# Performance work log

Measured on AMD Instinct MI355X. Metric: run time of the kernel, lower is better.

Reference implementation:

```python
import jax, jax.numpy as jnp
import numpy as np

D_MODEL = 1024
D_STATE = 16
D_CONV = 4
EXPAND = 2
D_INNER = EXPAND * D_MODEL
DT_RANK = (D_MODEL + 15) // 16  # ceil(d_model/16) = 64
BATCH = 2
SEQLEN = 1024


def _causal_conv_silu(x, w, b):
    # x: (B, d_inner, L); w: (d_inner, 1, k) depthwise; causal left padding k-1
    k = w.shape[-1]
    y = jax.lax.conv_general_dilated(
        x, w, window_strides=(1,), padding=[(k - 1, 0)],
        dimension_numbers=("NCH", "OIH", "NCH"), feature_group_count=x.shape[1])
    return jax.nn.silu(y + b[None, :, None])


def _ssm_scan(dA, dBx):
    # h_t = dA_t * h_{t-1} + dBx_t, parallel associative scan over L (axis=2)
    def op(e1, e2):
        a1, b1 = e1
        a2, b2 = e2
        return (a1 * a2, a2 * b1 + b2)
    return jax.lax.associative_scan(op, (dA, dBx), axis=2)[1]


def _mamba_dir(xz, conv_w, conv_b, xproj_w, dtproj_w, dt_bias, A_log, Dp):
    d_inner = xz.shape[1] // 2
    x, z = xz[:, :d_inner], xz[:, d_inner:]
    u = _causal_conv_silu(x, conv_w, conv_b)                  # (B, d, L)
    x_dbl = jnp.einsum('bdl,kd->bkl', u, xproj_w)             # (B, dt_rank+2n, L)
    n = A_log.shape[1]
    r = dtproj_w.shape[1]
    delta = jnp.einsum('dr,brl->bdl', dtproj_w, x_dbl[:, :r])
    Bm = x_dbl[:, r:r + n]                                    # (B, n, L)
    Cm = x_dbl[:, r + n:]                                     # (B, n, L)
    delta = jax.nn.softplus(delta + dt_bias[None, :, None])
    A = -jnp.exp(A_log)                                       # (d, n)
    dA = jnp.exp(jnp.einsum('bdl,dn->bdln', delta, A))
    dBx = jnp.einsum('bdl,bnl,bdl->bdln', delta, Bm, u)
    h = _ssm_scan(dA, dBx)                                    # (B, d, L, n)
    y = jnp.einsum('bdln,bnl->bdl', h, Cm)
    y = y + Dp[None, :, None] * u
    return y * jax.nn.silu(z)


def setup_inputs() -> dict:
    key = jax.random.key(0)
    ks = jax.random.split(key, 16)
    s_in = 1.0 / np.sqrt(D_MODEL)
    s_x = 1.0 / np.sqrt(D_INNER)
    dt_std = DT_RANK ** -0.5

    def dt_bias_init(k):
        dt = jnp.exp(jax.random.uniform(k, (D_INNER,)) * (np.log(0.1) - np.log(0.001)) + np.log(0.001))
        dt = jnp.clip(dt, 1e-4, None)
        return dt + jnp.log(-jnp.expm1(-dt))  # inverse softplus

    A_log = jnp.log(jnp.tile(jnp.arange(1, D_STATE + 1, dtype=jnp.float32)[None, :], (D_INNER, 1)))
    inp = {
        'hidden_states': jax.random.normal(ks[0], (BATCH, SEQLEN, D_MODEL), jnp.float32),
        'in_proj_w': jax.random.normal(ks[1], (2 * D_INNER, D_MODEL), jnp.float32) * s_in,
        'conv_w': jax.random.normal(ks[2], (D_INNER, 1, D_CONV), jnp.float32) * 0.3,
        'conv_bias': jnp.zeros((D_INNER,), jnp.float32),
        'x_proj_w': jax.random.normal(ks[3], (DT_RANK + 2 * D_STATE, D_INNER), jnp.float32) * s_x,
        'dt_proj_w': jax.random.uniform(ks[4], (D_INNER, DT_RANK), jnp.float32, -dt_std, dt_std),
        'dt_proj_bias': dt_bias_init(ks[5]),
        'A_log': A_log,
        'D_skip': jnp.ones((D_INNER,), jnp.float32),
        'convb_w': jax.random.normal(ks[6], (D_INNER, 1, D_CONV), jnp.float32) * 0.3,
        'convb_bias': jnp.zeros((D_INNER,), jnp.float32),
        'x_proj_b_w': jax.random.normal(ks[7], (DT_RANK + 2 * D_STATE, D_INNER), jnp.float32) * s_x,
        'dt_proj_b_w': jax.random.uniform(ks[8], (D_INNER, DT_RANK), jnp.float32, -dt_std, dt_std),
        'dt_proj_b_bias': dt_bias_init(ks[9]),
        'A_b_log': A_log,
        'D_b_skip': jnp.ones((D_INNER,), jnp.float32),
        'out_proj_w': jax.random.normal(ks[10], (D_MODEL, D_INNER), jnp.float32) * s_x,
    }
    return inp


def reference(hidden_states, in_proj_w, conv_w, conv_bias, x_proj_w, dt_proj_w,
              dt_proj_bias, A_log, D_skip, convb_w, convb_bias, x_proj_b_w,
              dt_proj_b_w, dt_proj_b_bias, A_b_log, D_b_skip, out_proj_w):
    # in_proj (no bias): (B, 2*d_inner, L)
    xz = jnp.einsum('ed,bld->bel', in_proj_w, hidden_states)
    out_f = _mamba_dir(xz, conv_w, conv_bias, x_proj_w, dt_proj_w, dt_proj_bias, A_log, D_skip)
    out_b = _mamba_dir(xz[:, :, ::-1], convb_w, convb_bias, x_proj_b_w, dt_proj_b_w,
                       dt_proj_b_bias, A_b_log, D_b_skip)[:, :, ::-1]
    # if_divide_out=False: just sum then out_proj (no bias)
    return jnp.einsum('bdl,od->blo', out_f + out_b, out_proj_w)
```

## Files before the change

### kernel.cpp

```cpp
#include <hip/hip_runtime.h>
#include <math.h>


typedef _Float16 f16x8 __attribute__((ext_vector_type(8)));
typedef _Float16 f16x4 __attribute__((ext_vector_type(4)));
typedef float    f32x4 __attribute__((ext_vector_type(4)));

#define SCH 16
#define SCL 64

__device__ __forceinline__ void gload_lds16(const void* g, void* l) {
    __builtin_amdgcn_global_load_lds(
        (const __attribute__((address_space(1))) void*)g,
        (__attribute__((address_space(3))) void*)l, 16, 0, 0);
}

__device__ __forceinline__ float softplus_f(float x) {
    float e = __builtin_amdgcn_exp2f(-fabsf(x) * 1.44269504f);
    return fmaxf(x, 0.f) + __builtin_amdgcn_logf(1.f + e) * 0.69314718f;
}

template<int CTRL>
__device__ __forceinline__ float dpp_add(float x) {
    int s = __builtin_amdgcn_update_dpp(0, __builtin_bit_cast(int, x),
                                        CTRL, 0xF, 0xF, true);
    return x + __builtin_bit_cast(float, s);
}

template<int WMW, int WNW, int FM, int FN>
__global__ __launch_bounds__(256)
void gemm_nt_f16(const _Float16* __restrict__ A, const _Float16* __restrict__ B,
                 float* __restrict__ C, int K, int ldc, long sA, long sC)
{
    constexpr int BM = WMW * FM * 16, BN = WNW * FN * 16;
    constexpr int ACH = BM / 8, NCH = (BM + BN) / 8;
    __shared__ __align__(16) _Float16 lds[(BM + BN) * 64];
    A += (long)blockIdx.z * sA;
    C += (long)blockIdx.z * sC;
    const int m0 = blockIdx.y * BM, n0 = blockIdx.x * BN;
    const int t = threadIdx.x, wid = t >> 6, lane = t & 63;
    const int wm = wid / WNW, wn = wid % WNW;
    const int srow = lane >> 3;
    const int skk  = ((lane & 7) ^ srow) * 8;

    f32x4 acc[FM][FN];
#pragma unroll
    for (int i = 0; i < FM; ++i)
#pragma unroll
        for (int j = 0; j < FN; ++j) acc[i][j] = (f32x4){0.f, 0.f, 0.f, 0.f};

    for (int k0 = 0; k0 < K; k0 += 64) {
#pragma unroll
        for (int c = wid; c < NCH; c += 4) {
            const _Float16* gp = (c < ACH)
                ? A + (long)(m0 + c * 8 + srow) * K + k0 + skk
                : B + (long)(n0 + (c - ACH) * 8 + srow) * K + k0 + skk;
            gload_lds16(gp, lds + c * 512);
        }
        __syncthreads();
#pragma unroll
        for (int kw = 0; kw < 2; ++kw) {
            f16x8 af[FM], bf[FN];
#pragma unroll
            for (int i = 0; i < FM; ++i) {
                int r = wm * FM * 16 + i * 16 + (lane & 15);
                af[i] = *(const f16x8*)(lds + r * 64 +
                        (((kw * 4 + (lane >> 4)) ^ (r & 7)) * 8));
            }
#pragma unroll
            for (int j = 0; j < FN; ++j) {
                int r = wn * FN * 16 + j * 16 + (lane & 15);
                bf[j] = *(const f16x8*)(lds + BM * 64 + r * 64 +
                        (((kw * 4 + (lane >> 4)) ^ (r & 7)) * 8));
            }
#pragma unroll
            for (int i = 0; i < FM; ++i)
#pragma unroll
                for (int j = 0; j < FN; ++j)
                    acc[i][j] = __builtin_amdgcn_mfma_f32_16x16x32_f16(
                        af[i], bf[j], acc[i][j], 0, 0, 0);
        }
        __syncthreads();
    }
#pragma unroll
    for (int i = 0; i < FM; ++i)
#pragma unroll
        for (int j = 0; j < FN; ++j) {
            int n = n0 + wn * FN * 16 + j * 16 + (lane & 15);
            int m = m0 + wm * FM * 16 + i * 16 + (lane >> 4) * 4;
            *(f32x4*)&C[(long)n * ldc + m] = acc[i][j];
        }
}

#define XP_SK 8
__global__ __launch_bounds__(256)
void xproj_f16_kernel(const float* __restrict__ u, const _Float16* __restrict__ xw16,
                      float* __restrict__ pb)
{
    __shared__ __align__(16) _Float16 Asw[128 * 64];
    __shared__ __align__(16) _Float16 Bsw[96 * 64];
    const int t = threadIdx.x, wid = t >> 6, lane = t & 63;
    const int wm = wid >> 1, wn = wid & 1;
    const int m0 = blockIdx.x * 128;
    const int sk = blockIdx.y, dirb = blockIdx.z;
    const float* ub = u + (long)dirb * 2048 * 1024;
    const _Float16* Bw = xw16 + (long)(dirb >> 1) * 96 * 2048;
    const int srow = lane >> 3;
    const int skk  = ((lane & 7) ^ srow) * 8;
    const int lloc = (t & 31) * 4;
    const int kslt = t >> 5;

    f32x4 acc[4][3];
#pragma unroll
    for (int i = 0; i < 4; ++i)
#pragma unroll
        for (int j = 0; j < 3; ++j) acc[i][j] = (f32x4){0.f, 0.f, 0.f, 0.f};

    for (int ks = 0; ks < 2048 / XP_SK; ks += 64) {
        const int k0 = sk * (2048 / XP_SK) + ks;
#pragma unroll
        for (int c = wid; c < 12; c += 4)
            gload_lds16(Bw + (long)(c * 8 + srow) * 2048 + k0 + skk, Bsw + c * 512);
        float av[8][4];
#pragma unroll
        for (int kk = 0; kk < 8; ++kk) {
            f32x4 v = *(const f32x4*)&ub[(long)(k0 + kslt * 8 + kk) * 1024 + m0 + lloc];
            av[kk][0] = v.x; av[kk][1] = v.y; av[kk][2] = v.z; av[kk][3] = v.w;
        }
#pragma unroll
        for (int q = 0; q < 4; ++q) {
            int l = lloc + q;
            f16x8 h = {(_Float16)av[0][q], (_Float16)av[1][q], (_Float16)av[2][q],
                       (_Float16)av[3][q], (_Float16)av[4][q], (_Float16)av[5][q],
                       (_Float16)av[6][q], (_Float16)av[7][q]};
            *(f16x8*)(Asw + l * 64 + ((kslt ^ (l & 7)) * 8)) = h;
        }
        __syncthreads();
#pragma unroll
        for (int kw = 0; kw < 2; ++kw) {
            f16x8 af[4], bf[3];
#pragma unroll
            for (int i = 0; i < 4; ++i) {
                int r = wm * 64 + i * 16 + (lane & 15);
                af[i] = *(const f16x8*)(Asw + r * 64 +
                        (((kw * 4 + (lane >> 4)) ^ (r & 7)) * 8));
            }
#pragma unroll
            for (int j = 0; j < 3; ++j) {
                int r = wn * 48 + j * 16 + (lane & 15);
                bf[j] = *(const f16x8*)(Bsw + r * 64 +
                        (((kw * 4 + (lane >> 4)) ^ (r & 7)) * 8));
            }
#pragma unroll
            for (int i = 0; i < 4; ++i)
#pragma unroll
                for (int j = 0; j < 3; ++j)
                    acc[i][j] = __builtin_amdgcn_mfma_f32_16x16x32_f16(
                        af[i], bf[j], acc[i][j], 0, 0, 0);
        }
        __syncthreads();
    }
    float* Cp = pb + ((long)sk * 4 + dirb) * 96 * 1024;
#pragma unroll
    for (int i = 0; i < 4; ++i)
#pragma unroll
        for (int j = 0; j < 3; ++j) {
            int n = wn * 48 + j * 16 + (lane & 15);
            int m = m0 + wm * 64 + i * 16 + (lane >> 4) * 4;
            *(f32x4*)&Cp[(long)n * 1024 + m] = acc[i][j];
        }
}

__global__ __launch_bounds__(256)
void xreduce_kernel(const float* __restrict__ pb, float* __restrict__ xdbl)
{
    int f = (blockIdx.x * 256 + threadIdx.x) * 4;
    f32x4 s = (f32x4){0.f, 0.f, 0.f, 0.f};
#pragma unroll
    for (int sk = 0; sk < XP_SK; ++sk)
        s += *(const f32x4*)(pb + (long)sk * 393216 + f);
    *(f32x4*)(xdbl + f) = s;
}

__global__ __launch_bounds__(256)
void dtproj_f16_kernel(const float* __restrict__ xdbl, const _Float16* __restrict__ dw16,
                       const float* __restrict__ bcat, float* __restrict__ delta)
{
    __shared__ __align__(16) _Float16 Asw[128 * 64];
    __shared__ __align__(16) _Float16 Bsw[128 * 64];
    const int t = threadIdx.x, wid = t >> 6, lane = t & 63;
    const int wm = wid >> 1, wn = wid & 1;
    const int n0 = blockIdx.x * 128, m0 = blockIdx.y * 128;
    const int dirb = blockIdx.z, dir = dirb >> 1;
    const float* Xb = xdbl + (long)dirb * 96 * 1024;
    const _Float16* Bw = dw16 + (long)dir * 2048 * 64;
    const int srow = lane >> 3, skk = ((lane & 7) ^ srow) * 8;
    const int lloc = (t & 31) * 4, kslt = t >> 5;

#pragma unroll
    for (int c = wid; c < 16; c += 4)
        gload_lds16(Bw + (long)(n0 + c * 8 + srow) * 64 + skk, Bsw + c * 512);
    float av[8][4];
#pragma unroll
    for (int kk = 0; kk < 8; ++kk) {
        f32x4 v = *(const f32x4*)&Xb[(long)(kslt * 8 + kk) * 1024 + m0 + lloc];
        av[kk][0] = v.x; av[kk][1] = v.y; av[kk][2] = v.z; av[kk][3] = v.w;
    }
#pragma unroll
    for (int q = 0; q < 4; ++q) {
        int l = lloc + q;
        f16x8 h = {(_Float16)av[0][q], (_Float16)av[1][q], (_Float16)av[2][q],
                   (_Float16)av[3][q], (_Float16)av[4][q], (_Float16)av[5][q],
                   (_Float16)av[6][q], (_Float16)av[7][q]};
        *(f16x8*)(Asw + l * 64 + ((kslt ^ (l & 7)) * 8)) = h;
    }
    __syncthreads();

    f32x4 acc[4][4];
#pragma unroll
    for (int i = 0; i < 4; ++i)
#pragma unroll
        for (int j = 0; j < 4; ++j) acc[i][j] = (f32x4){0.f, 0.f, 0.f, 0.f};
#pragma unroll
    for (int kw = 0; kw < 2; ++kw) {
        f16x8 af[4], bf[4];
#pragma unroll
        for (int i = 0; i < 4; ++i) {
            int r = wm * 64 + i * 16 + (lane & 15);
            af[i] = *(const f16x8*)(Asw + r * 64 +
                    (((kw * 4 + (lane >> 4)) ^ (r & 7)) * 8));
        }
#pragma unroll
        for (int j = 0; j < 4; ++j) {
            int r = wn * 64 + j * 16 + (lane & 15);
            bf[j] = *(const f16x8*)(Bsw + r * 64 +
                    (((kw * 4 + (lane >> 4)) ^ (r & 7)) * 8));
        }
#pragma unroll
        for (int i = 0; i < 4; ++i)
#pragma unroll
            for (int j = 0; j < 4; ++j)
                acc[i][j] = __builtin_amdgcn_mfma_f32_16x16x32_f16(
                    af[i], bf[j], acc[i][j], 0, 0, 0);
    }
    float* Dp = delta + (long)dirb * 2048 * 1024;
#pragma unroll
    for (int j = 0; j < 4; ++j) {
        int dd = n0 + wn * 64 + j * 16 + (lane & 15);
        float bm = bcat[dir * 2048 + dd];
#pragma unroll
        for (int i = 0; i < 4; ++i) {
            int m = m0 + wm * 64 + i * 16 + (lane >> 4) * 4;
            f32x4 v = acc[i][j];
            f32x4 o = {softplus_f(v.x + bm), softplus_f(v.y + bm),
                       softplus_f(v.z + bm), softplus_f(v.w + bm)};
            *(f32x4*)&Dp[(long)dd * 1024 + m] = o;
        }
    }
}

__global__ __launch_bounds__(256)
void cvt_f16_kernel(const float* __restrict__ in, _Float16* __restrict__ out, int n)
{
    int i = (blockIdx.x * 256 + threadIdx.x) * 4;
    if (i + 3 < n) {
        float4 v = *(const float4*)(in + i);
        f16x4 h = {(_Float16)v.x, (_Float16)v.y, (_Float16)v.z, (_Float16)v.w};
        *(f16x4*)(out + i) = h;
    }
}

__global__ __launch_bounds__(256)
void concat_weights(const float* __restrict__ xwf, const float* __restrict__ xwb,
                    const float* __restrict__ dwf, const float* __restrict__ dwb,
                    const float* __restrict__ bf,  const float* __restrict__ bb,
                    _Float16* __restrict__ xw16, _Float16* __restrict__ dw16,
                    float* __restrict__ bcat)
{
    int i = blockIdx.x * 256 + threadIdx.x;
    if (i < 196608) { xw16[i] = (_Float16)xwf[i]; xw16[196608 + i] = (_Float16)xwb[i]; }
    if (i < 131072) { dw16[i] = (_Float16)dwf[i]; dw16[131072 + i] = (_Float16)dwb[i]; }
    if (i < 2048)   { bcat[i]  = bf[i];  bcat[2048 + i] = bb[i]; }
}

__global__ __launch_bounds__(256)
void conv_silu_kernel(const float* __restrict__ xz,
                      const float* __restrict__ wf, const float* __restrict__ bf,
                      const float* __restrict__ wb, const float* __restrict__ bbk,
                      float* __restrict__ u)
{
    long idx = (long)blockIdx.x * 256 + threadIdx.x;
    int l = (int)(idx & 1023);
    long r = idx >> 10;
    int d = (int)(r & 2047);
    int b = (int)((r >> 11) & 1);
    int dir = (int)(r >> 12);
    const float* x = xz + ((long)b * 4096 + d) * 1024;
    const float* w = dir ? wb : wf;
    float s = dir ? bbk[d] : bf[d];
    if (dir == 0) {
#pragma unroll
        for (int j = 0; j < 4; ++j) {
            int p = l - 3 + j;
            if (p >= 0) s = fmaf(w[d * 4 + j], x[p], s);
        }
    } else {
#pragma unroll
        for (int j = 0; j < 4; ++j) {
            int src = l - 3 + j;
            if (src >= 0) s = fmaf(w[d * 4 + j], x[1023 - src], s);
        }
    }
    u[idx] = s / (1.f + __builtin_amdgcn_exp2f(-s * 1.44269504f));
}

__global__ __launch_bounds__(256)
void scan_p1_kernel(const float* __restrict__ u, const float* __restrict__ delta,
                    const float* __restrict__ xdbl,
                    const float* __restrict__ Alf, const float* __restrict__ Alb,
                    float* __restrict__ hend, float* __restrict__ aprod)
{
    __shared__ float sD[64][66], sU[64][66], sB[64][20];
    const int t = threadIdx.x, wid = t >> 6, lane = t & 63;
    const int nl = lane & 3;
    const int dloc = wid * 16 + (lane >> 2);
    const int dblk = blockIdx.x, chunk = blockIdx.y, dirb = blockIdx.z;
    const int d = dblk * 64 + dloc, dir = dirb >> 1;
    const int T0 = chunk * SCL;
    f32x4 Av = *(const f32x4*)((dir ? Alb : Alf) + d * 16 + nl * 4);
    float An2[4] = {-expf(Av.x) * 1.44269504f, -expf(Av.y) * 1.44269504f,
                    -expf(Av.z) * 1.44269504f, -expf(Av.w) * 1.44269504f};
    const float* dp = delta + ((long)dirb * 2048 + dblk * 64) * 1024;
    const float* up = u     + ((long)dirb * 2048 + dblk * 64) * 1024;
    const float* Bp = xdbl  + ((long)dirb * 96 + 64) * 1024;

#pragma unroll
    for (int rep = 0; rep < 4; ++rep) {
        int ii = rep * 256 + t;
        int dd = ii >> 4, q = ii & 15;
        *(f32x4*)&sD[dd][q * 4] = *(const f32x4*)&dp[(long)dd * 1024 + T0 + q * 4];
        *(f32x4*)&sU[dd][q * 4] = *(const f32x4*)&up[(long)dd * 1024 + T0 + q * 4];
    }
#pragma unroll
    for (int rep = 0; rep < 4; ++rep) {
        int ii = rep * 256 + t;
        int n = ii >> 6, tt = ii & 63;
        sB[tt][n] = Bp[(long)n * 1024 + T0 + tt];
    }
    __syncthreads();

    float h[4] = {0.f, 0.f, 0.f, 0.f};
    float S = 0.f;
#pragma unroll 4
    for (int g = 0; g < 16; ++g) {
        f32x4 dlv = *(const f32x4*)&sD[dloc][g * 4];
        f32x4 uuv = *(const f32x4*)&sU[dloc][g * 4];
        float dls[4] = {dlv.x, dlv.y, dlv.z, dlv.w};
        float uus[4] = {uuv.x, uuv.y, uuv.z, uuv.w};
#pragma unroll
        for (int r4 = 0; r4 < 4; ++r4) {
            f32x4 Bv = *(const f32x4*)&sB[g * 4 + r4][nl * 4];
            float Bs[4] = {Bv.x, Bv.y, Bv.z, Bv.w};
            float dl = dls[r4], t1 = dl * uus[r4];
            S += dl;
#pragma unroll
            for (int r = 0; r < 4; ++r)
                h[r] = fmaf(__builtin_amdgcn_exp2f(dl * An2[r]), h[r], t1 * Bs[r]);
        }
    }
    long cb = (((long)dirb * SCH + chunk) * 2048 + d) * 16 + nl * 4;
    *(f32x4*)&hend[cb]  = (f32x4){h[0], h[1], h[2], h[3]};
    *(f32x4*)&aprod[cb] = (f32x4){__builtin_amdgcn_exp2f(S * An2[0]),
                                  __builtin_amdgcn_exp2f(S * An2[1]),
                                  __builtin_amdgcn_exp2f(S * An2[2]),
                                  __builtin_amdgcn_exp2f(S * An2[3])};
}

__global__ __launch_bounds__(256)
void scan_carry_kernel(const float* __restrict__ hend, const float* __restrict__ aprod,
                       float* __restrict__ hinit)
{
    int f = blockIdx.x * 256 + threadIdx.x;
    int dn = f & 32767;
    int dirb = f >> 15;
    long base = (long)dirb * SCH * 32768 + dn;
    float hcur = 0.f;
#pragma unroll
    for (int c = 0; c < SCH; ++c) {
        hinit[base + (long)c * 32768] = hcur;
        hcur = hend[base + (long)c * 32768]
             + aprod[base + (long)c * 32768] * hcur;
    }
}

__global__ __launch_bounds__(256)
void scan_p3_kernel(const float* __restrict__ u, const float* __restrict__ delta,
                    const float* __restrict__ xdbl,
                    const float* __restrict__ Alf, const float* __restrict__ Alb,
                    const float* __restrict__ Df, const float* __restrict__ Db,
                    const float* __restrict__ hinit, float* __restrict__ y)
{
    __shared__ float sD[64][66], sU[64][66], sB[64][20], sC[64][20];
    const int t = threadIdx.x, wid = t >> 6, lane = t & 63;
    const int nl = lane & 3;
    const int dloc = wid * 16 + (lane >> 2);
    const int dblk = blockIdx.x, chunk = blockIdx.y, dirb = blockIdx.z;
    const int d = dblk * 64 + dloc, dir = dirb >> 1;
    const int T0 = chunk * SCL;
    f32x4 Av = *(const f32x4*)((dir ? Alb : Alf) + d * 16 + nl * 4);
    float An2[4] = {-expf(Av.x) * 1.44269504f, -expf(Av.y) * 1.44269504f,
                    -expf(Av.z) * 1.44269504f, -expf(Av.w) * 1.44269504f};
    const float Dd = (dir ? Db : Df)[d];
    const float* dp = delta + ((long)dirb * 2048 + dblk * 64) * 1024;
    const float* up = u     + ((long)dirb * 2048 + dblk * 64) * 1024;
    const float* Bp = xdbl  + ((long)dirb * 96 + 64) * 1024;
    const float* Cp = xdbl  + ((long)dirb * 96 + 80) * 1024;
    float* yrow = y + ((long)dirb * 2048 + d) * 1024;

#pragma unroll
    for (int rep = 0; rep < 4; ++rep) {
        int ii = rep * 256 + t;
        int dd = ii >> 4, q = ii & 15;
        *(f32x4*)&sD[dd][q * 4] = *(const f32x4*)&dp[(long)dd * 1024 + T0 + q * 4];
        *(f32x4*)&sU[dd][q * 4] = *(const f32x4*)&up[(long)dd * 1024 + T0 + q * 4];
    }
#pragma unroll
    for (int rep = 0; rep < 4; ++rep) {
        int ii = rep * 256 + t;
        int n = ii >> 6, tt = ii & 63;
        sB[tt][n] = Bp[(long)n * 1024 + T0 + tt];
        sC[tt][n] = Cp[(long)n * 1024 + T0 + tt];
    }
    long cb = (((long)dirb * SCH + chunk) * 2048 + d) * 16 + nl * 4;
    f32x4 h0v = *(const f32x4*)&hinit[cb];
    float h[4] = {h0v.x, h0v.y, h0v.z, h0v.w};
    const bool m[4] = {nl == 0, nl == 1, nl == 2, nl == 3};
    __syncthreads();

#pragma unroll 4
    for (int g = 0; g < 16; ++g) {
        f32x4 dlv = *(const f32x4*)&sD[dloc][g * 4];
        f32x4 uuv = *(const f32x4*)&sU[dloc][g * 4];
        float dls[4] = {dlv.x, dlv.y, dlv.z, dlv.w};
        float uus[4] = {uuv.x, uuv.y, uuv.z, uuv.w};
        float keep = 0.f;
#pragma unroll
        for (int r4 = 0; r4 < 4; ++r4) {
            f32x4 Bv = *(const f32x4*)&sB[g * 4 + r4][nl * 4];
            f32x4 Cv = *(const f32x4*)&sC[g * 4 + r4][nl * 4];
            float Bs[4] = {Bv.x, Bv.y, Bv.z, Bv.w};
            float Cs[4] = {Cv.x, Cv.y, Cv.z, Cv.w};
            float dl = dls[r4], uu = uus[r4];
            float t1 = dl * uu;
#pragma unroll
            for (int r = 0; r < 4; ++r)
                h[r] = fmaf(__builtin_amdgcn_exp2f(dl * An2[r]), h[r], t1 * Bs[r]);
            float p = h[0] * Cs[0];
            p = fmaf(h[1], Cs[1], p);
            p = fmaf(h[2], Cs[2], p);
            p = fmaf(h[3], Cs[3], p);
            p = dpp_add<0xB1>(p);
            p = dpp_add<0x4E>(p);
            float fy = fmaf(Dd, uu, p);
            keep = m[r4] ? fy : keep;
        }
        yrow[T0 + g * 4 + nl] = keep;
    }
}

__global__ __launch_bounds__(256)
void combine_T_kernel(const float* __restrict__ xz, const float* __restrict__ y,
                      _Float16* __restrict__ GT)
{
    __shared__ float Ls[64][65];
    const int d0 = blockIdx.x * 64, l0 = blockIdx.y * 64, b = blockIdx.z;
    const int t = threadIdx.x;
#pragma unroll
    for (int rep = 0; rep < 4; ++rep) {
        int i = rep * 256 + t;
        int dl = i >> 4;
        int lq = (i & 15) * 4;
        const float* zp  = xz + ((long)b * 4096 + 2048 + d0 + dl) * 1024 + l0 + lq;
        const float* yfp = y  + ((long)(b)     * 2048 + d0 + dl) * 1024 + l0 + lq;
        const float* ybp = y  + ((long)(2 + b) * 2048 + d0 + dl) * 1024 + (1020 - l0 - lq);
        float4 vz = *(const float4*)zp;
        float4 vf = *(const float4*)yfp;
        float4 vb = *(const float4*)ybp;
        float zz[4]  = {vz.x, vz.y, vz.z, vz.w};
        float ff[4]  = {vf.x, vf.y, vf.z, vf.w};
        float bbv[4] = {vb.w, vb.z, vb.y, vb.x};
#pragma unroll
        for (int qq = 0; qq < 4; ++qq) {
            float z = zz[qq];
            float sz = z / (1.f + __builtin_amdgcn_exp2f(-z * 1.44269504f));
            Ls[dl][lq + qq] = sz * (ff[qq] + bbv[qq]);
        }
    }
    __syncthreads();
#pragma unroll
    for (int rep = 0; rep < 4; ++rep) {
        int i = rep * 256 + t;
        int ll = i >> 4;
        int dq = (i & 15) * 4;
        f16x4 h = {(_Float16)Ls[dq][ll], (_Float16)Ls[dq + 1][ll],
                   (_Float16)Ls[dq + 2][ll], (_Float16)Ls[dq + 3][ll]};
        *(f16x4*)(GT + ((long)(b * 1024 + l0 + ll)) * 2048 + d0 + dq) = h;
    }
}

extern "C" void kernel_launch(void* const* d_in, const int* in_sizes, int n_in,
                              void* d_out, int out_size, void* d_ws, size_t ws_size,
                              hipStream_t stream)
{
    const float* hidden   = (const float*)d_in[0];
    const float* inproj_w = (const float*)d_in[1];
    const float* conv_w   = (const float*)d_in[2];
    const float* conv_b   = (const float*)d_in[3];
    const float* xproj_w  = (const float*)d_in[4];
    const float* dtproj_w = (const float*)d_in[5];
    const float* dt_bias  = (const float*)d_in[6];
    const float* A_log    = (const float*)d_in[7];
    const float* D_skip   = (const float*)d_in[8];
    const float* convb_w  = (const float*)d_in[9];
    const float* convb_b  = (const float*)d_in[10];
    const float* xprojb_w = (const float*)d_in[11];
    const float* dtprojb_w= (const float*)d_in[12];
    const float* dtb_bias = (const float*)d_in[13];
    const float* Ab_log   = (const float*)d_in[14];
    const float* Db_skip  = (const float*)d_in[15];
    const float* outproj_w= (const float*)d_in[16];
    float* out = (float*)d_out;

    float* ws    = (float*)d_ws;
    float* xz    = ws;
    float* u     = ws + 8388608;
    float* xdbl  = ws + 16777216;
    float* delta = ws + 17170432;
    float* y     = ws + 25559040;
    _Float16* H16    = (_Float16*)u;
    _Float16* Win16  = (_Float16*)(u + 1048576);
    float*    xpb    = delta;
    _Float16* GT     = (_Float16*)delta;
    _Float16* Wout16 = (_Float16*)y;
    _Float16* dw16   = (_Float16*)y;
    float*    bcat   = y + 131072;
    _Float16* xw16   = (_Float16*)(y + 135168);
    float* hend  = y;
    float* aprod = y + 2097152;
    float* hinit = xz;

    hipLaunchKernelGGL(cvt_f16_kernel, dim3(2048), dim3(256), 0, stream,
        hidden, H16, 2097152);
    hipLaunchKernelGGL(cvt_f16_kernel, dim3(4096), dim3(256), 0, stream,
        inproj_w, Win16, 4194304);

    hipLaunchKernelGGL(concat_weights, dim3(768), dim3(256), 0, stream,
        xproj_w, xprojb_w, dtproj_w, dtprojb_w, dt_bias, dtb_bias,
        xw16, dw16, bcat);

    hipLaunchKernelGGL((gemm_nt_f16<2, 2, 4, 4>),
        dim3(32, 8, 2), dim3(256), 0, stream,
        H16, Win16, xz, 1024, 1024, 1048576L, 4194304L);

    hipLaunchKernelGGL(conv_silu_kernel, dim3(32768), dim3(256), 0, stream,
        xz, conv_w, conv_b, convb_w, convb_b, u);

    hipLaunchKernelGGL(xproj_f16_kernel, dim3(8, XP_SK, 4), dim3(256), 0, stream,
        u, xw16, xpb);
    hipLaunchKernelGGL(xreduce_kernel, dim3(384), dim3(256), 0, stream,
        xpb, xdbl);

    hipLaunchKernelGGL(dtproj_f16_kernel, dim3(16, 8, 4), dim3(256), 0, stream,
        xdbl, dw16, bcat, delta);

    hipLaunchKernelGGL(scan_p1_kernel, dim3(32, SCH, 4), dim3(256), 0, stream,
        u, delta, xdbl, A_log, Ab_log, hend, aprod);
    hipLaunchKernelGGL(scan_carry_kernel, dim3(512), dim3(256), 0, stream,
        hend, aprod, hinit);
    hipLaunchKernelGGL(scan_p3_kernel, dim3(32, SCH, 4), dim3(256), 0, stream,
        u, delta, xdbl, A_log, Ab_log, D_skip, Db_skip, hinit, y);

    hipLaunchKernelGGL(combine_T_kernel, dim3(32, 16, 2), dim3(256), 0, stream,
        xz, y, GT);

    hipLaunchKernelGGL(cvt_f16_kernel, dim3(2048), dim3(256), 0, stream,
        outproj_w, Wout16, 2097152);

    hipLaunchKernelGGL((gemm_nt_f16<4, 1, 2, 4>),
        dim3(32, 8, 1), dim3(256), 0, stream,
        Wout16, GT, out, 2048, 1024, 0L, 0L);
}
```

Measured before the change: 199.0 us.

## Process two channels per thread in scan kernels to boost ILP and reuse

```diff
diff --git a/kernel.cpp b/kernel.cpp
--- a/kernel.cpp
+++ b/kernel.cpp
@@ -320,22 +320,27 @@
                     const float* __restrict__ Alf, const float* __restrict__ Alb,
                     float* __restrict__ hend, float* __restrict__ aprod)
 {
-    __shared__ float sD[64][66], sU[64][66], sB[64][20];
+    __shared__ float sD[128][68], sU[128][68], sB[64][20];
     const int t = threadIdx.x, wid = t >> 6, lane = t & 63;
     const int nl = lane & 3;
-    const int dloc = wid * 16 + (lane >> 2);
+    const int da = wid * 32 + (lane >> 2);
+    const int db = da + 16;
     const int dblk = blockIdx.x, chunk = blockIdx.y, dirb = blockIdx.z;
-    const int d = dblk * 64 + dloc, dir = dirb >> 1;
+    const int dir = dirb >> 1;
     const int T0 = chunk * SCL;
-    f32x4 Av = *(const f32x4*)((dir ? Alb : Alf) + d * 16 + nl * 4);
-    float An2[4] = {-expf(Av.x) * 1.44269504f, -expf(Av.y) * 1.44269504f,
-                    -expf(Av.z) * 1.44269504f, -expf(Av.w) * 1.44269504f};
-    const float* dp = delta + ((long)dirb * 2048 + dblk * 64) * 1024;
-    const float* up = u     + ((long)dirb * 2048 + dblk * 64) * 1024;
+    const float* Al = (dir ? Alb : Alf) + (long)dblk * 128 * 16;
+    f32x4 Ava = *(const f32x4*)(Al + da * 16 + nl * 4);
+    f32x4 Avb = *(const f32x4*)(Al + db * 16 + nl * 4);
+    float Aa[4] = {-expf(Ava.x) * 1.44269504f, -expf(Ava.y) * 1.44269504f,
+                   -expf(Ava.z) * 1.44269504f, -expf(Ava.w) * 1.44269504f};
+    float Ab[4] = {-expf(Avb.x) * 1.44269504f, -expf(Avb.y) * 1.44269504f,
+                   -expf(Avb.z) * 1.44269504f, -expf(Avb.w) * 1.44269504f};
+    const float* dp = delta + ((long)dirb * 2048 + dblk * 128) * 1024;
+    const float* up = u     + ((long)dirb * 2048 + dblk * 128) * 1024;
     const float* Bp = xdbl  + ((long)dirb * 96 + 64) * 1024;
 
 #pragma unroll
-    for (int rep = 0; rep < 4; ++rep) {
+    for (int rep = 0; rep < 8; ++rep) {
         int ii = rep * 256 + t;
         int dd = ii >> 4, q = ii & 15;
         *(f32x4*)&sD[dd][q * 4] = *(const f32x4*)&dp[(long)dd * 1024 + T0 + q * 4];
@@ -349,31 +354,44 @@
     }
     __syncthreads();
 
-    float h[4] = {0.f, 0.f, 0.f, 0.f};
-    float S = 0.f;
+    float ha[4] = {0.f, 0.f, 0.f, 0.f}, hb[4] = {0.f, 0.f, 0.f, 0.f};
+    float Sa = 0.f, Sb = 0.f;
 #pragma unroll 4
     for (int g = 0; g < 16; ++g) {
-        f32x4 dlv = *(const f32x4*)&sD[dloc][g * 4];
-        f32x4 uuv = *(const f32x4*)&sU[dloc][g * 4];
-        float dls[4] = {dlv.x, dlv.y, dlv.z, dlv.w};
-        float uus[4] = {uuv.x, uuv.y, uuv.z, uuv.w};
+        f32x4 dla = *(const f32x4*)&sD[da][g * 4];
+        f32x4 uua = *(const f32x4*)&sU[da][g * 4];
+        f32x4 dlb = *(const f32x4*)&sD[db][g * 4];
+        f32x4 uub = *(const f32x4*)&sU[db][g * 4];
+        float dlsa[4] = {dla.x, dla.y, dla.z, dla.w};
+        float uusa[4] = {uua.x, uua.y, uua.z, uua.w};
+        float dlsb[4] = {dlb.x, dlb.y, dlb.z, dlb.w};
+        float uusb[4] = {uub.x, uub.y, uub.z, uub.w};
 #pragma unroll
         for (int r4 = 0; r4 < 4; ++r4) {
             f32x4 Bv = *(const f32x4*)&sB[g * 4 + r4][nl * 4];
             float Bs[4] = {Bv.x, Bv.y, Bv.z, Bv.w};
-            float dl = dls[r4], t1 = dl * uus[r4];
-            S += dl;
-#pragma unroll
-            for (int r = 0; r < 4; ++r)
-                h[r] = fmaf(__builtin_amdgcn_exp2f(dl * An2[r]), h[r], t1 * Bs[r]);
-        }
-    }
-    long cb = (((long)dirb * SCH + chunk) * 2048 + d) * 16 + nl * 4;
-    *(f32x4*)&hend[cb]  = (f32x4){h[0], h[1], h[2], h[3]};
-    *(f32x4*)&aprod[cb] = (f32x4){__builtin_amdgcn_exp2f(S * An2[0]),
-                                  __builtin_amdgcn_exp2f(S * An2[1]),
-                                  __builtin_amdgcn_exp2f(S * An2[2]),
-                                  __builtin_amdgcn_exp2f(S * An2[3])};
+            float d1 = dlsa[r4], t1 = d1 * uusa[r4];
+            float d2 = dlsb[r4], t2 = d2 * uusb[r4];
+            Sa += d1; Sb += d2;
+#pragma unroll
+            for (int r = 0; r < 4; ++r) {
+                ha[r] = fmaf(__builtin_amdgcn_exp2f(d1 * Aa[r]), ha[r], t1 * Bs[r]);
+                hb[r] = fmaf(__builtin_amdgcn_exp2f(d2 * Ab[r]), hb[r], t2 * Bs[r]);
+            }
+        }
+    }
+    long cba = (((long)dirb * SCH + chunk) * 2048 + dblk * 128 + da) * 16 + nl * 4;
+    long cbb = (((long)dirb * SCH + chunk) * 2048 + dblk * 128 + db) * 16 + nl * 4;
+    *(f32x4*)&hend[cba]  = (f32x4){ha[0], ha[1], ha[2], ha[3]};
+    *(f32x4*)&hend[cbb]  = (f32x4){hb[0], hb[1], hb[2], hb[3]};
+    *(f32x4*)&aprod[cba] = (f32x4){__builtin_amdgcn_exp2f(Sa * Aa[0]),
+                                   __builtin_amdgcn_exp2f(Sa * Aa[1]),
+                                   __builtin_amdgcn_exp2f(Sa * Aa[2]),
+                                   __builtin_amdgcn_exp2f(Sa * Aa[3])};
+    *(f32x4*)&aprod[cbb] = (f32x4){__builtin_amdgcn_exp2f(Sb * Ab[0]),
+                                   __builtin_amdgcn_exp2f(Sb * Ab[1]),
+                                   __builtin_amdgcn_exp2f(Sb * Ab[2]),
+                                   __builtin_amdgcn_exp2f(Sb * Ab[3])};
 }
 
 __global__ __launch_bounds__(256)
@@ -400,25 +418,32 @@
                     const float* __restrict__ Df, const float* __restrict__ Db,
                     const float* __restrict__ hinit, float* __restrict__ y)
 {
-    __shared__ float sD[64][66], sU[64][66], sB[64][20], sC[64][20];
+    __shared__ float sD[128][68], sU[128][68], sB[64][20], sC[64][20];
     const int t = threadIdx.x, wid = t >> 6, lane = t & 63;
     const int nl = lane & 3;
-    const int dloc = wid * 16 + (lane >> 2);
+    const int da = wid * 32 + (lane >> 2);
+    const int db = da + 16;
     const int dblk = blockIdx.x, chunk = blockIdx.y, dirb = blockIdx.z;
-    const int d = dblk * 64 + dloc, dir = dirb >> 1;
+    const int dir = dirb >> 1;
     const int T0 = chunk * SCL;
-    f32x4 Av = *(const f32x4*)((dir ? Alb : Alf) + d * 16 + nl * 4);
-    float An2[4] = {-expf(Av.x) * 1.44269504f, -expf(Av.y) * 1.44269504f,
-                    -expf(Av.z) * 1.44269504f, -expf(Av.w) * 1.44269504f};
-    const float Dd = (dir ? Db : Df)[d];
-    const float* dp = delta + ((long)dirb * 2048 + dblk * 64) * 1024;
-    const float* up = u     + ((long)dirb * 2048 + dblk * 64) * 1024;
+    const float* Al = (dir ? Alb : Alf) + (long)dblk * 128 * 16;
+    f32x4 Ava = *(const f32x4*)(Al + da * 16 + nl * 4);
+    f32x4 Avb = *(const f32x4*)(Al + db * 16 + nl * 4);
+    float Aa[4] = {-expf(Ava.x) * 1.44269504f, -expf(Ava.y) * 1.44269504f,
+                   -expf(Ava.z) * 1.44269504f, -expf(Ava.w) * 1.44269504f};
+    float Ab[4] = {-expf(Avb.x) * 1.44269504f, -expf(Avb.y) * 1.44269504f,
+                   -expf(Avb.z) * 1.44269504f, -expf(Avb.w) * 1.44269504f};
+    const float Dda = (dir ? Db : Df)[dblk * 128 + da];
+    const float Ddb = (dir ? Db : Df)[dblk * 128 + db];
+    const float* dp = delta + ((long)dirb * 2048 + dblk * 128) * 1024;
+    const float* up = u     + ((long)dirb * 2048 + dblk * 128) * 1024;
     const float* Bp = xdbl  + ((long)dirb * 96 + 64) * 1024;
     const float* Cp = xdbl  + ((long)dirb * 96 + 80) * 1024;
-    float* yrow = y + ((long)dirb * 2048 + d) * 1024;
-
-#pragma unroll
-    for (int rep = 0; rep < 4; ++rep) {
+    float* yra = y + ((long)dirb * 2048 + dblk * 128 + da) * 1024;
+    float* yrb = y + ((long)dirb * 2048 + dblk * 128 + db) * 1024;
+
+#pragma unroll
+    for (int rep = 0; rep < 8; ++rep) {
         int ii = rep * 256 + t;
         int dd = ii >> 4, q = ii & 15;
         *(f32x4*)&sD[dd][q * 4] = *(const f32x4*)&dp[(long)dd * 1024 + T0 + q * 4];
@@ -431,40 +456,58 @@
         sB[tt][n] = Bp[(long)n * 1024 + T0 + tt];
         sC[tt][n] = Cp[(long)n * 1024 + T0 + tt];
     }
-    long cb = (((long)dirb * SCH + chunk) * 2048 + d) * 16 + nl * 4;
-    f32x4 h0v = *(const f32x4*)&hinit[cb];
-    float h[4] = {h0v.x, h0v.y, h0v.z, h0v.w};
+    long cba = (((long)dirb * SCH + chunk) * 2048 + dblk * 128 + da) * 16 + nl * 4;
+    long cbb = (((long)dirb * SCH + chunk) * 2048 + dblk * 128 + db) * 16 + nl * 4;
+    f32x4 h0a = *(const f32x4*)&hinit[cba];
+    f32x4 h0b = *(const f32x4*)&hinit[cbb];
+    float ha[4] = {h0a.x, h0a.y, h0a.z, h0a.w};
+    float hb[4] = {h0b.x, h0b.y, h0b.z, h0b.w};
     const bool m[4] = {nl == 0, nl == 1, nl == 2, nl == 3};
     __syncthreads();
 
 #pragma unroll 4
     for (int g = 0; g < 16; ++g) {
-        f32x4 dlv = *(const f32x4*)&sD[dloc][g * 4];
-        f32x4 uuv = *(const f32x4*)&sU[dloc][g * 4];
-        float dls[4] = {dlv.x, dlv.y, dlv.z, dlv.w};
-        float uus[4] = {uuv.x, uuv.y, uuv.z, uuv.w};
-        float keep = 0.f;
+        f32x4 dla = *(const f32x4*)&sD[da][g * 4];
+        f32x4 uua = *(const f32x4*)&sU[da][g * 4];
+        f32x4 dlb = *(const f32x4*)&sD[db][g * 4];
+        f32x4 uub = *(const f32x4*)&sU[db][g * 4];
+        float dlsa[4] = {dla.x, dla.y, dla.z, dla.w};
+        float uusa[4] = {uua.x, uua.y, uua.z, uua.w};
+        float dlsb[4] = {dlb.x, dlb.y, dlb.z, dlb.w};
+        float uusb[4] = {uub.x, uub.y, uub.z, uub.w};
+        float keepa = 0.f, keepb = 0.f;
 #pragma unroll
         for (int r4 = 0; r4 < 4; ++r4) {
             f32x4 Bv = *(const f32x4*)&sB[g * 4 + r4][nl * 4];
             f32x4 Cv = *(const f32x4*)&sC[g * 4 + r4][nl * 4];
             float Bs[4] = {Bv.x, Bv.y, Bv.z, Bv.w};
             float Cs[4] = {Cv.x, Cv.y, Cv.z, Cv.w};
-            float dl = dls[r4], uu = uus[r4];
-            float t1 = dl * uu;
-#pragma unroll
-            for (int r = 0; r < 4; ++r)
-                h[r] = fmaf(__builtin_amdgcn_exp2f(dl * An2[r]), h[r], t1 * Bs[r]);
-            float p = h[0] * Cs[0];
-            p = fmaf(h[1], Cs[1], p);
-            p = fmaf(h[2], Cs[2], p);
-            p = fmaf(h[3], Cs[3], p);
-            p = dpp_add<0xB1>(p);
-            p = dpp_add<0x4E>(p);
-            float fy = fmaf(Dd, uu, p);
-            keep = m[r4] ? fy : keep;
-        }
-        yrow[T0 + g * 4 + nl] = keep;
+            float d1 = dlsa[r4], u1 = uusa[r4], t1 = d1 * u1;
+            float d2 = dlsb[r4], u2 = uusb[r4], t2 = d2 * u2;
+#pragma unroll
+            for (int r = 0; r < 4; ++r) {
+                ha[r] = fmaf(__builtin_amdgcn_exp2f(d1 * Aa[r]), ha[r], t1 * Bs[r]);
+                hb[r] = fmaf(__builtin_amdgcn_exp2f(d2 * Ab[r]), hb[r], t2 * Bs[r]);
+            }
+            float pa = ha[0] * Cs[0];
+            pa = fmaf(ha[1], Cs[1], pa);
+            pa = fmaf(ha[2], Cs[2], pa);
+            pa = fmaf(ha[3], Cs[3], pa);
+            float pb2 = hb[0] * Cs[0];
+            pb2 = fmaf(hb[1], Cs[1], pb2);
+            pb2 = fmaf(hb[2], Cs[2], pb2);
+            pb2 = fmaf(hb[3], Cs[3], pb2);
+            pa  = dpp_add<0xB1>(pa);
+            pa  = dpp_add<0x4E>(pa);
+            pb2 = dpp_add<0xB1>(pb2);
+            pb2 = dpp_add<0x4E>(pb2);
+            float fya = fmaf(Dda, u1, pa);
+            float fyb = fmaf(Ddb, u2, pb2);
+            keepa = m[r4] ? fya : keepa;
+            keepb = m[r4] ? fyb : keepb;
+        }
+        yra[T0 + g * 4 + nl] = keepa;
+        yrb[T0 + g * 4 + nl] = keepb;
     }
 }
 
@@ -573,11 +616,11 @@
     hipLaunchKernelGGL(dtproj_f16_kernel, dim3(16, 8, 4), dim3(256), 0, stream,
         xdbl, dw16, bcat, delta);
 
-    hipLaunchKernelGGL(scan_p1_kernel, dim3(32, SCH, 4), dim3(256), 0, stream,
+    hipLaunchKernelGGL(scan_p1_kernel, dim3(16, SCH, 4), dim3(256), 0, stream,
         u, delta, xdbl, A_log, Ab_log, hend, aprod);
     hipLaunchKernelGGL(scan_carry_kernel, dim3(512), dim3(256), 0, stream,
         hend, aprod, hinit);
-    hipLaunchKernelGGL(scan_p3_kernel, dim3(32, SCH, 4), dim3(256), 0, stream,
+    hipLaunchKernelGGL(scan_p3_kernel, dim3(16, SCH, 4), dim3(256), 0, stream,
         u, delta, xdbl, A_log, Ab_log, D_skip, Db_skip, hinit, y);
 
     hipLaunchKernelGGL(combine_T_kernel, dim3(32, 16, 2), dim3(256), 0, stream,
```

Measured after the change: 228.7 us. 15.0% more time.
